# Performance work log

Measured on AMD Instinct MI355X. Metric: run time of the kernel, lower is better.

Reference implementation:

```python
import jax, jax.numpy as jnp
import numpy as np

T, B, IN_DIM, H, NB = 100, 1024, 40, 512, 4
WB, IB, ABMVM, ABNM = 8, 8, 8, 8


def _pact(x, a):
    # PACT clip sign(x)*min(|x|, a); a: (NB,) broadcast over (NB, B, D)
    a = a[:, None, None]
    return jnp.sign(x) * 0.5 * (jnp.abs(x) - jnp.abs(jnp.abs(x) - a) + a)


def _quant(x, bits, rng):
    step = 2.0 ** (bits - 1)
    x01 = jnp.clip(x / rng, -1.0 + 1.0 / step, 1.0 - 1.0 / step)
    return jnp.round(x01 * step) / step * rng


def _q(x, bits, a):
    # straight-through quantizer with per-block range a: (NB,)
    return x + jax.lax.stop_gradient(_quant(x, bits, a[:, None, None]) - x)


@jax.custom_vjp
def custom_mm(x, w, b):
    wc = jnp.clip(w, -1.0, 1.0)
    return jnp.einsum('nbi,nio->nbo', x, _quant(wc, WB, 1.0)) + _quant(b, WB, 1.0)


def _mm_fwd(x, w, b):
    wc = jnp.clip(w, -1.0, 1.0)
    out = jnp.einsum('nbi,nio->nbo', x, _quant(wc, WB, 1.0)) + _quant(b, WB, 1.0)
    return out, (x, wc)


def _mm_bwd(res, g):
    x, wc = res
    return (jnp.einsum('nbo,nio->nbi', g, wc),
            jnp.einsum('nbi,nbo->nio', x, g),
            g.sum(axis=1, keepdims=True))


custom_mm.defvjp(_mm_fwd, _mm_bwd)


def _forward(inputs, weight_ih, weight_hh, bias_ih, bias_hh, a_cell, fc_w, fc_b, fc_a):
    (a1, a2, a3, a4, a5, a6, a7, a8, a9,
     a10, a11, a12, a13, a14) = a_cell
    nb, hd = weight_hh.shape[0], weight_hh.shape[1]
    bsz = inputs.shape[1]

    def step(carry, x_t):
        hx, cx = carry
        xr = jnp.broadcast_to(x_t[None], (nb,) + x_t.shape)  # input.repeat(n_blocks,1,1)
        p1 = custom_mm(_q(_pact(xr, a1), IB, a1), weight_ih, bias_ih)
        p2 = custom_mm(_q(_pact(hx, a11), IB, a11), weight_hh, bias_hh)  # w_mask == ones (drop_p=0)
        pre = _q(_pact(p1, a12), ABMVM, a12) + _q(_pact(p2, a13), ABMVM, a13)
        gates = _q(_pact(pre, a14), ABNM, a14)  # (nb, B, 4H)
        i, j, f, o = jnp.split(gates, 4, axis=2)
        fg = _q(_pact(jax.nn.sigmoid(f), a3), ABNM, a3)
        ig = _q(_pact(jax.nn.sigmoid(i), a4), ABNM, a4)
        jg = _q(_pact(jnp.tanh(j), a5), ABNM, a5)
        og = _q(_pact(jax.nn.sigmoid(o), a6), ABNM, a6)
        gc = _q(_pact(cx * fg, a7), ABNM, a7)
        ai = _q(_pact(ig * jg, a8), ABNM, a8)
        nc = _q(_pact(gc + ai, a9), ABNM, a9)
        ac = _q(_pact(jnp.tanh(nc), a10), ABNM, a10)
        nh = _q(_pact(ac * og, a11), ABNM, a11)
        return (nh, nc), None

    h0 = jnp.zeros((nb, bsz, hd), inputs.dtype)
    (hT, _), _ = jax.lax.scan(step, (h0, h0), inputs)
    fa1, fa2 = fc_a
    fc = _q(_pact(custom_mm(_q(_pact(hT, fa1), IB, fa1), fc_w, fc_b), fa2), ABMVM, fa2)  # (nb, B, 3)
    return fc[:4].transpose(1, 0, 2).reshape(bsz, 12)


def setup_inputs():
    key = jax.random.key(0)
    k = jax.random.split(key, 4)
    lim_ih = 1.0 / np.sqrt(IN_DIM)
    lim_hh = 1.0 / np.sqrt(H)
    lim_fc = np.sqrt(6.0 / H)
    a_vals = jnp.array([128., 16., 1., 1., 1., 1., 4., 1., 4., 1., 4., 4., 4., 4.], jnp.float32)
    return {
        "inputs": jax.random.normal(k[0], (T, B, IN_DIM), jnp.float32),
        "weight_ih": jax.random.uniform(k[1], (NB, IN_DIM, 4 * H), jnp.float32, -lim_ih, lim_ih),
        "weight_hh": jax.random.uniform(k[2], (NB, H, 4 * H), jnp.float32, -lim_hh, lim_hh),
        "bias_ih": jnp.zeros((NB, 1, 4 * H), jnp.float32),
        "bias_hh": jnp.ones((NB, 1, 4 * H), jnp.float32),
        "a_cell": jnp.broadcast_to(a_vals[:, None], (14, NB)),
        "fc_w": jax.random.uniform(k[3], (NB, H, 3), jnp.float32, -lim_fc, lim_fc),
        "fc_b": jnp.zeros((NB, 1, 3), jnp.float32),
        "fc_a": jnp.broadcast_to(jnp.array([4., 16.], jnp.float32)[:, None], (2, NB)),
    }


def reference(inputs, weight_ih, weight_hh, bias_ih, bias_hh, a_cell, fc_w, fc_b, fc_a):
    return _forward(inputs, weight_ih, weight_hh, bias_ih, bias_hh, a_cell, fc_w, fc_b, fc_a)
```

## Files before the change

kernel.cpp:

```cpp
#include <hip/hip_runtime.h>
#include <math.h>

#define T_STEPS 100
#define BATCH   1024
#define INDIM   40
#define HID     512
#define NBLK    4
#define KPAD    576
#define NG      2048
#define LDAP    80

typedef int v4i __attribute__((ext_vector_type(4)));

__device__ __forceinline__ float pact_f(float x, float a){
    float u = fabsf(x);
    float v = fabsf(u - a);
    float s = (x > 0.f) ? 1.f : ((x < 0.f) ? -1.f : 0.f);
    return (s * 0.5f) * ((u - v) + a);
}
__device__ __forceinline__ int quant_int(float x, float inv_a){
    float xs = x * inv_a;
    xs = fminf(fmaxf(xs, -127.f/128.f), 127.f/128.f);
    return (int)rintf(xs * 128.f);
}
__device__ __forceinline__ int clamp127(int v){
    return v > 127 ? 127 : (v < -127 ? -127 : v);
}

__global__ __launch_bounds__(256) void k_quant_x(const float* __restrict__ x,
                                                 signed char* __restrict__ xq){
    int idx = blockIdx.x * 256 + threadIdx.x;
    int k = idx & 63; int tb = idx >> 6;
    signed char q = 0;
    if (k < INDIM){
        float xv = x[tb * INDIM + k];
        float pv = pact_f(xv, 128.f);
        q = (signed char)quant_int(pv, 1.f/128.f);
    }
    xq[idx] = q;
}

__global__ __launch_bounds__(256) void k_quant_w(const float* __restrict__ wih,
                                                 const float* __restrict__ whh,
                                                 signed char* __restrict__ wt){
    int idx = blockIdx.x * 256 + threadIdx.x;
    int kk = idx % KPAD;
    int no = idx / KPAD;
    int c  = no % NG;
    int n  = no / NG;
    int gate = (c >> 4) & 3;
    int h    = ((c >> 6) << 4) | (c & 15);
    int o    = gate * 512 + h;
    float w;
    if (kk < INDIM)      w = wih[((long)n*INDIM + kk)*NG + o];
    else if (kk < 64)    { wt[idx] = 0; return; }
    else                 w = whh[((long)n*HID + (kk-64))*NG + o];
    w = fminf(fmaxf(w, -1.f), 1.f);
    wt[idx] = (signed char)quant_int(w, 1.f);
}

__global__ __launch_bounds__(256) void k_quant_bias(const float* __restrict__ bih,
                                                    const float* __restrict__ bhh,
                                                    int* __restrict__ bihq,
                                                    int* __restrict__ bhhq){
    int idx = blockIdx.x * 256 + threadIdx.x;
    int c = idx % NG; int n = idx / NG;
    int gate = (c >> 4) & 3;
    int h    = ((c >> 6) << 4) | (c & 15);
    int o    = gate * 512 + h;
    bihq[idx] = quant_int(bih[n*NG + o], 1.f);
    bhhq[idx] = quant_int(bhh[n*NG + o], 1.f);
}

__global__ __launch_bounds__(256) void k_quant_fc(const float* __restrict__ fcw,
                                                  const float* __restrict__ fcb,
                                                  signed char* __restrict__ fcwt,
                                                  int* __restrict__ fcbq){
    int idx = blockIdx.x * 256 + threadIdx.x;
    if (idx < NBLK*3*512){
        int k = idx % 512; int nc = idx / 512; int c = nc % 3; int n = nc / 3;
        float w = fcw[((long)n*HID + k)*3 + c];
        w = fminf(fmaxf(w, -1.f), 1.f);
        fcwt[idx] = (signed char)quant_int(w, 1.f);
    }
    if (idx < NBLK*3) fcbq[idx] = quant_int(fcb[idx], 1.f);
}

__global__ void k_luts(signed char* __restrict__ sigl, signed char* __restrict__ thl){
    int i = threadIdx.x;
    if (i < 255){
        double xv = (double)(i - 127) / 32.0;
        float s = (float)(1.0 / (1.0 + exp(-xv)));
        float t = (float)tanh(xv);
        sigl[i] = (signed char)quant_int(pact_f(s, 1.f), 1.f);
        thl[i]  = (signed char)quant_int(pact_f(t, 1.f), 1.f);
    }
}

__global__ __launch_bounds__(256, 2) void k_step(const signed char* __restrict__ xq_t,
                                                 const signed char* __restrict__ Hin,
                                                 signed char* __restrict__ Hout,
                                                 signed char* __restrict__ C,
                                                 const signed char* __restrict__ Wt,
                                                 const int* __restrict__ bihq,
                                                 const int* __restrict__ bhhq,
                                                 const signed char* __restrict__ sigl,
                                                 const signed char* __restrict__ thl){
    __shared__ __align__(16) signed char As[128*LDAP];
    __shared__ __align__(16) signed char Bs[128*LDAP];
    __shared__ signed char s_sig[256], s_th[256];

    int lid = blockIdx.x;
    int swz = (lid & 7) * 64 + (lid >> 3);
    int bm = swz & 7, bn = (swz >> 3) & 15, n = swz >> 7;

    int tid  = threadIdx.x;
    int lane = tid & 63;
    int wave = tid >> 6;
    int wm = wave >> 1, wn = wave & 1;

    if (tid < 255){ s_sig[tid] = sigl[tid]; s_th[tid] = thl[tid]; }

    int hglob = bn*32 + wn*16 + (lane & 15);
    int rbase = bm*128 + wm*64 + ((lane >> 4) << 2);

    int cbase = bn*128 + wn*64 + (lane & 15);
    int b1v[4], b2v[4];
    #pragma unroll
    for (int ni = 0; ni < 4; ++ni){
        int c = cbase + ni*16;
        b1v[ni] = bihq[n*NG + c];
        b2v[ni] = 32 * bhhq[n*NG + c];
    }
    int* Cw = (int*)(C + ((long)(n*HID + hglob))*BATCH + rbase);
    int cold[4];
    #pragma unroll
    for (int mi = 0; mi < 4; ++mi) cold[mi] = Cw[mi*4];

    int sr = tid >> 2;
    int sc = (tid & 3) * 16;
    const signed char* wr0 = Wt  + (long)n*NG*KPAD   + (long)(bn*128 + sr)*KPAD + sc;
    const signed char* wr1 = wr0 + (long)64*KPAD;
    const signed char* hr0 = Hin + (long)n*BATCH*HID + (long)(bm*128 + sr)*HID  + sc;
    const signed char* hr1 = hr0 + (long)64*HID;
    int wlo = sr*LDAP + (tid & 3)*16;
    int whi = wlo + 64*LDAP;

    int4 ra0 = *(const int4*)(xq_t + (long)bm*8192 + tid*16);
    int4 ra1 = *(const int4*)(xq_t + (long)bm*8192 + 4096 + tid*16);
    int4 rb0 = *(const int4*)(wr0);
    int4 rb1 = *(const int4*)(wr1);

    v4i acc1[4][4] = {};
    v4i acc2[4][4] = {};
    int am = wm*64 + (lane & 15);
    int bo = wn*64 + (lane & 15);
    int ak = (lane >> 4) * 16;

    for (int kt = 0; kt < 9; ++kt){
        __syncthreads();
        *(int4*)&As[wlo] = ra0; *(int4*)&As[whi] = ra1;
        *(int4*)&Bs[wlo] = rb0; *(int4*)&Bs[whi] = rb1;
        __syncthreads();
        if (kt < 8){
            ra0 = *(const int4*)(hr0 + kt*64);
            ra1 = *(const int4*)(hr1 + kt*64);
            rb0 = *(const int4*)(wr0 + (kt+1)*64);
            rb1 = *(const int4*)(wr1 + (kt+1)*64);
        }
        v4i af[4], bf[4];
        #pragma unroll
        for (int mi = 0; mi < 4; ++mi) af[mi] = *(const v4i*)&As[(am + mi*16)*LDAP + ak];
        #pragma unroll
        for (int ni = 0; ni < 4; ++ni) bf[ni] = *(const v4i*)&Bs[(bo + ni*16)*LDAP + ak];
        if (kt == 0){
            #pragma unroll
            for (int mi = 0; mi < 4; ++mi)
                #pragma unroll
                for (int ni = 0; ni < 4; ++ni)
                    acc1[mi][ni] = __builtin_amdgcn_mfma_i32_16x16x64_i8(af[mi], bf[ni], acc1[mi][ni], 0, 0, 0);
        } else {
            #pragma unroll
            for (int mi = 0; mi < 4; ++mi)
                #pragma unroll
                for (int ni = 0; ni < 4; ++ni)
                    acc2[mi][ni] = __builtin_amdgcn_mfma_i32_16x16x64_i8(af[mi], bf[ni], acc2[mi][ni], 0, 0, 0);
        }
    }

    long hb = (long)n * BATCH;
    #pragma unroll
    for (int mi = 0; mi < 4; ++mi){
        int cw = cold[mi];
        int cnew = 0;
        #pragma unroll
        for (int r = 0; r < 4; ++r){
            int g4[4];
            #pragma unroll
            for (int ni = 0; ni < 4; ++ni){
                int S1  = acc1[mi][ni][r] + b1v[ni];
                int q12 = clamp127((int)rintf((float)S1 * 0.25f));
                int S2  = acc2[mi][ni][r] + b2v[ni];
                int q13 = clamp127((int)rintf((float)S2 * 0.0078125f));
                g4[ni]  = clamp127(q12 + q13);
            }
            int ig = s_sig[g4[0] + 127];
            int jg = s_th [g4[1] + 127];
            int fg = s_sig[g4[2] + 127];
            int og = s_sig[g4[3] + 127];
            int cc = (signed char)(cw >> (8*r));
            int gc = clamp127((int)rintf((float)(cc * fg) * 0.0078125f));
            int ai = clamp127((int)rintf((float)(ig * jg) * 0.0078125f));
            int nc = clamp127((int)rintf((float)(4*gc + ai) * 0.25f));
            int ac = s_th[nc + 127];
            int nh = clamp127((int)rintf((float)(ac * og) * (1.0f/512.0f)));
            cnew |= (nc & 255) << (8*r);
            Hout[(hb + rbase + mi*16 + r)*HID + hglob] = (signed char)nh;
        }
        Cw[mi*4] = cnew;
    }
}

__global__ __launch_bounds__(256) void k_fc(const signed char* __restrict__ H,
                                            const signed char* __restrict__ fcwt,
                                            const int* __restrict__ fcbq,
                                            float* __restrict__ out){
    int wave = threadIdx.x >> 6, lane = threadIdx.x & 63;
    int nb = blockIdx.x * 4 + wave;
    int n = nb >> 10, b = nb & 1023;
    const signed char* h = H + (long)nb * HID + lane * 8;
    int2 hv = *(const int2*)h;
    int acc[3] = {0, 0, 0};
    #pragma unroll
    for (int c = 0; c < 3; ++c){
        const signed char* wp = fcwt + ((long)(n*3 + c))*512 + lane*8;
        int2 wv = *(const int2*)wp;
        int s = 0;
        #pragma unroll
        for (int e = 0; e < 4; ++e){
            s += (int)(signed char)(hv.x >> (8*e)) * (int)(signed char)(wv.x >> (8*e));
            s += (int)(signed char)(hv.y >> (8*e)) * (int)(signed char)(wv.y >> (8*e));
        }
        acc[c] = s;
    }
    #pragma unroll
    for (int off = 32; off; off >>= 1){
        acc[0] += __shfl_down(acc[0], off, 64);
        acc[1] += __shfl_down(acc[1], off, 64);
        acc[2] += __shfl_down(acc[2], off, 64);
    }
    if (lane == 0){
        #pragma unroll
        for (int c = 0; c < 3; ++c){
            int v = acc[c] + 32 * fcbq[n*3 + c];
            int q = clamp127((int)rintf((float)v * (1.0f/512.0f)));
            out[b*12 + n*3 + c] = (float)q * 0.125f;
        }
    }
}

extern "C" void kernel_launch(void* const* d_in, const int* in_sizes, int n_in,
                              void* d_out, int out_size, void* d_ws, size_t ws_size,
                              hipStream_t stream)
{
    const float* x   = (const float*)d_in[0];
    const float* wih = (const float*)d_in[1];
    const float* whh = (const float*)d_in[2];
    const float* bih = (const float*)d_in[3];
    const float* bhh = (const float*)d_in[4];
    const float* fcw = (const float*)d_in[6];
    const float* fcb = (const float*)d_in[7];
    float* out = (float*)d_out;
    (void)in_sizes; (void)n_in; (void)out_size; (void)ws_size;

    char* p = (char*)d_ws;
    auto alloc = [&](size_t nbytes){ char* r = p; p += (nbytes + 255) & ~(size_t)255; return r; };
    signed char* Xq   = (signed char*)alloc((size_t)T_STEPS*BATCH*64);
    signed char* Wt   = (signed char*)alloc((size_t)NBLK*NG*KPAD);
    signed char* Hb0  = (signed char*)alloc((size_t)NBLK*BATCH*HID);
    signed char* Hb1  = (signed char*)alloc((size_t)NBLK*BATCH*HID);
    signed char* Cb   = (signed char*)alloc((size_t)NBLK*BATCH*HID);
    int*         bihq = (int*)alloc((size_t)NBLK*NG*4);
    int*         bhhq = (int*)alloc((size_t)NBLK*NG*4);
    signed char* fcwt = (signed char*)alloc((size_t)NBLK*3*512);
    int*         fcbq = (int*)alloc((size_t)NBLK*3*4);
    signed char* sigl = (signed char*)alloc(256);
    signed char* thl  = (signed char*)alloc(256);

    k_quant_x   <<<(T_STEPS*BATCH*64)/256, 256, 0, stream>>>(x, Xq);
    k_quant_w   <<<(NBLK*NG*KPAD)/256,     256, 0, stream>>>(wih, whh, Wt);
    k_quant_bias<<<(NBLK*NG)/256,          256, 0, stream>>>(bih, bhh, bihq, bhhq);
    k_quant_fc  <<<(NBLK*3*512)/256,       256, 0, stream>>>(fcw, fcb, fcwt, fcbq);
    k_luts      <<<1, 256, 0, stream>>>(sigl, thl);
    hipMemsetAsync(Hb0, 0, (size_t)3*NBLK*BATCH*HID, stream);

    for (int t = 0; t < T_STEPS; ++t){
        const signed char* Hi = (t & 1) ? Hb1 : Hb0;
        signed char*       Ho = (t & 1) ? Hb0 : Hb1;
        k_step<<<512, 256, 0, stream>>>(Xq + (size_t)t*BATCH*64, Hi, Ho, Cb, Wt, bihq, bhhq, sigl, thl);
    }
    k_fc<<<(NBLK*BATCH)/4, 256, 0, stream>>>(Hb0, fcwt, fcbq, out);
}
```

Measured before the change: 1.428 ms.

## Replace per-timestep launches with persistent kernel holding weights in LDS and grid barrier

Replaces the 100 per-timestep kernel launches with one persistent kernel of 256 blocks. Each block loads its 128-column weight panel into shared memory once, keeps the cell state in registers instead of global memory, and synchronises timesteps with a global atomic counter barrier. This removes launch overhead, the repeated weight reloads and the C-state round trips. In exchange it depends on all 256 blocks being co-resident for the spin barrier and uses about 117KB of LDS per block. The H tile is double-buffered in LDS.

```diff
diff --git a/kernel.cpp b/kernel.cpp
--- a/kernel.cpp
+++ b/kernel.cpp
@@ -9,6 +9,10 @@
 #define KPAD    576
 #define NG      2048
 #define LDAP    80
+#define LDWP    592
+#define SMEM_WS 75776
+#define SMEM_AS 20480
+#define SMEM_TOTAL (SMEM_WS + 2*SMEM_AS + 512)
 
 typedef int v4i __attribute__((ext_vector_type(4)));
 
@@ -97,127 +101,169 @@
     }
 }
 
-__global__ __launch_bounds__(256, 2) void k_step(const signed char* __restrict__ xq_t,
-                                                 const signed char* __restrict__ Hin,
-                                                 signed char* __restrict__ Hout,
-                                                 signed char* __restrict__ C,
-                                                 const signed char* __restrict__ Wt,
-                                                 const int* __restrict__ bihq,
-                                                 const int* __restrict__ bhhq,
-                                                 const signed char* __restrict__ sigl,
-                                                 const signed char* __restrict__ thl){
-    __shared__ __align__(16) signed char As[128*LDAP];
-    __shared__ __align__(16) signed char Bs[128*LDAP];
-    __shared__ signed char s_sig[256], s_th[256];
-
-    int lid = blockIdx.x;
-    int swz = (lid & 7) * 64 + (lid >> 3);
-    int bm = swz & 7, bn = (swz >> 3) & 15, n = swz >> 7;
+__global__ __launch_bounds__(512, 2) void k_persist(const signed char* __restrict__ Xq,
+                                                    signed char* __restrict__ H0,
+                                                    signed char* __restrict__ H1,
+                                                    const signed char* __restrict__ Wt,
+                                                    const int* __restrict__ bihq,
+                                                    const int* __restrict__ bhhq,
+                                                    const signed char* __restrict__ sigl,
+                                                    const signed char* __restrict__ thl,
+                                                    unsigned int* __restrict__ bar){
+    extern __shared__ char smem[];
+    signed char* Ws    = (signed char*)smem;
+    signed char* As    = (signed char*)(smem + SMEM_WS);
+    signed char* s_sig = (signed char*)(smem + SMEM_WS + 2*SMEM_AS);
+    signed char* s_th  = s_sig + 256;
 
     int tid  = threadIdx.x;
     int lane = tid & 63;
     int wave = tid >> 6;
     int wm = wave >> 1, wn = wave & 1;
 
+    int bid  = blockIdx.x;
+    int xcd  = bid & 7, slot = bid >> 3;
+    int gidx = xcd * 2 + (slot >> 4);
+    int n    = gidx >> 2;
+    int bmq  = gidx & 3;
+    int bn   = slot & 15;
+
+    const signed char* wpan = Wt + ((long)n*NG + (long)bn*128) * KPAD;
+    for (int i = tid; i < 4608; i += 512){
+        int row = i / 36, c = (i % 36) * 16;
+        *(int4*)&Ws[row*LDWP + c] = *(const int4*)(wpan + (long)row*KPAD + c);
+    }
     if (tid < 255){ s_sig[tid] = sigl[tid]; s_th[tid] = thl[tid]; }
 
     int hglob = bn*32 + wn*16 + (lane & 15);
-    int rbase = bm*128 + wm*64 + ((lane >> 4) << 2);
-
+    int rbase = bmq*256 + wm*64 + ((lane >> 4) << 2);
     int cbase = bn*128 + wn*64 + (lane & 15);
     int b1v[4], b2v[4];
     #pragma unroll
     for (int ni = 0; ni < 4; ++ni){
-        int c = cbase + ni*16;
-        b1v[ni] = bihq[n*NG + c];
-        b2v[ni] = 32 * bhhq[n*NG + c];
-    }
-    int* Cw = (int*)(C + ((long)(n*HID + hglob))*BATCH + rbase);
-    int cold[4];
-    #pragma unroll
-    for (int mi = 0; mi < 4; ++mi) cold[mi] = Cw[mi*4];
-
-    int sr = tid >> 2;
-    int sc = (tid & 3) * 16;
-    const signed char* wr0 = Wt  + (long)n*NG*KPAD   + (long)(bn*128 + sr)*KPAD + sc;
-    const signed char* wr1 = wr0 + (long)64*KPAD;
-    const signed char* hr0 = Hin + (long)n*BATCH*HID + (long)(bm*128 + sr)*HID  + sc;
-    const signed char* hr1 = hr0 + (long)64*HID;
-    int wlo = sr*LDAP + (tid & 3)*16;
-    int whi = wlo + 64*LDAP;
-
-    int4 ra0 = *(const int4*)(xq_t + (long)bm*8192 + tid*16);
-    int4 ra1 = *(const int4*)(xq_t + (long)bm*8192 + 4096 + tid*16);
-    int4 rb0 = *(const int4*)(wr0);
-    int4 rb1 = *(const int4*)(wr1);
-
-    v4i acc1[4][4] = {};
-    v4i acc2[4][4] = {};
+        b1v[ni] = bihq[n*NG + cbase + ni*16];
+        b2v[ni] = 32 * bhhq[n*NG + cbase + ni*16];
+    }
+    int cold[4] = {0,0,0,0};
+
+    int  srow = tid >> 1;
+    int  scol = (tid & 1) * 32;
+    int  aoff = srow*LDAP + scol;
+    long hoff = ((long)(n*BATCH + bmq*256 + srow)) * HID + scol;
+    const signed char* xb = Xq + (long)bmq*16384 + srow*64 + scol;
+
     int am = wm*64 + (lane & 15);
-    int bo = wn*64 + (lane & 15);
     int ak = (lane >> 4) * 16;
-
-    for (int kt = 0; kt < 9; ++kt){
+    int bro = (wn*64 + (lane & 15)) * LDWP;
+
+    __syncthreads();
+
+    for (int t = 0; t < T_STEPS; ++t){
+        const signed char* Hin  = (t & 1) ? H1 : H0;
+        signed char*       Hout = (t & 1) ? H0 : H1;
+
+        const signed char* xp = xb + (long)t * (BATCH*64);
+        int4 rx0 = *(const int4*)xp;
+        int4 rx1 = *(const int4*)(xp + 16);
+
+        if (t){
+            __syncthreads();
+            if (tid == 0){
+                __builtin_amdgcn_fence(__ATOMIC_RELEASE, "agent");
+                atomicAdd(bar, 1u);
+                unsigned tgt = (unsigned)t * 256u;
+                while (__hip_atomic_load(bar, __ATOMIC_RELAXED, __HIP_MEMORY_SCOPE_AGENT) < tgt)
+                    __builtin_amdgcn_s_sleep(1);
+                __builtin_amdgcn_fence(__ATOMIC_ACQUIRE, "agent");
+            }
+            __syncthreads();
+        }
+
+        *(int4*)&As[aoff] = rx0; *(int4*)&As[aoff + 16] = rx1;
         __syncthreads();
-        *(int4*)&As[wlo] = ra0; *(int4*)&As[whi] = ra1;
-        *(int4*)&Bs[wlo] = rb0; *(int4*)&Bs[whi] = rb1;
-        __syncthreads();
-        if (kt < 8){
-            ra0 = *(const int4*)(hr0 + kt*64);
-            ra1 = *(const int4*)(hr1 + kt*64);
-            rb0 = *(const int4*)(wr0 + (kt+1)*64);
-            rb1 = *(const int4*)(wr1 + (kt+1)*64);
-        }
-        v4i af[4], bf[4];
-        #pragma unroll
-        for (int mi = 0; mi < 4; ++mi) af[mi] = *(const v4i*)&As[(am + mi*16)*LDAP + ak];
-        #pragma unroll
-        for (int ni = 0; ni < 4; ++ni) bf[ni] = *(const v4i*)&Bs[(bo + ni*16)*LDAP + ak];
-        if (kt == 0){
+        int4 ha0 = *(const int4*)(Hin + hoff);
+        int4 ha1 = *(const int4*)(Hin + hoff + 16);
+        int4 hb0 = *(const int4*)(Hin + hoff + 64);
+        int4 hb1 = *(const int4*)(Hin + hoff + 80);
+
+        v4i acc1[4][4] = {};
+        {
+            v4i af[4], bf[4];
+            #pragma unroll
+            for (int mi = 0; mi < 4; ++mi) af[mi] = *(const v4i*)&As[(am + mi*16)*LDAP + ak];
+            #pragma unroll
+            for (int ni = 0; ni < 4; ++ni) bf[ni] = *(const v4i*)&Ws[bro + ni*16*LDWP + ak];
             #pragma unroll
             for (int mi = 0; mi < 4; ++mi)
                 #pragma unroll
                 for (int ni = 0; ni < 4; ++ni)
                     acc1[mi][ni] = __builtin_amdgcn_mfma_i32_16x16x64_i8(af[mi], bf[ni], acc1[mi][ni], 0, 0, 0);
-        } else {
+        }
+        int q12p[4][4];
+        #pragma unroll
+        for (int mi = 0; mi < 4; ++mi)
+            #pragma unroll
+            for (int ni = 0; ni < 4; ++ni){
+                int p = 0;
+                #pragma unroll
+                for (int r = 0; r < 4; ++r){
+                    int q = clamp127((int)rintf((float)(acc1[mi][ni][r] + b1v[ni]) * 0.25f));
+                    p |= (q & 255) << (8*r);
+                }
+                q12p[mi][ni] = p;
+            }
+
+        v4i acc2[4][4] = {};
+        for (int kt = 1; kt <= 8; ++kt){
+            signed char* Ab = As + (kt & 1) * SMEM_AS;
+            *(int4*)&Ab[aoff] = ha0; *(int4*)&Ab[aoff + 16] = ha1;
+            __syncthreads();
+            ha0 = hb0; ha1 = hb1;
+            if (kt <= 6){
+                hb0 = *(const int4*)(Hin + hoff + (kt+1)*64);
+                hb1 = *(const int4*)(Hin + hoff + (kt+1)*64 + 16);
+            }
+            v4i af[4], bf[4];
+            #pragma unroll
+            for (int mi = 0; mi < 4; ++mi) af[mi] = *(const v4i*)&Ab[(am + mi*16)*LDAP + ak];
+            #pragma unroll
+            for (int ni = 0; ni < 4; ++ni) bf[ni] = *(const v4i*)&Ws[bro + ni*16*LDWP + kt*64 + ak];
             #pragma unroll
             for (int mi = 0; mi < 4; ++mi)
                 #pragma unroll
                 for (int ni = 0; ni < 4; ++ni)
                     acc2[mi][ni] = __builtin_amdgcn_mfma_i32_16x16x64_i8(af[mi], bf[ni], acc2[mi][ni], 0, 0, 0);
         }
-    }
-
-    long hb = (long)n * BATCH;
-    #pragma unroll
-    for (int mi = 0; mi < 4; ++mi){
-        int cw = cold[mi];
-        int cnew = 0;
+
         #pragma unroll
-        for (int r = 0; r < 4; ++r){
-            int g4[4];
-            #pragma unroll
-            for (int ni = 0; ni < 4; ++ni){
-                int S1  = acc1[mi][ni][r] + b1v[ni];
-                int q12 = clamp127((int)rintf((float)S1 * 0.25f));
-                int S2  = acc2[mi][ni][r] + b2v[ni];
-                int q13 = clamp127((int)rintf((float)S2 * 0.0078125f));
-                g4[ni]  = clamp127(q12 + q13);
+        for (int mi = 0; mi < 4; ++mi){
+            int cw = cold[mi];
+            int cnew = 0;
+            #pragma unroll
+            for (int r = 0; r < 4; ++r){
+                int g4[4];
+                #pragma unroll
+                for (int ni = 0; ni < 4; ++ni){
+                    int S2  = acc2[mi][ni][r] + b2v[ni];
+                    int q13 = clamp127((int)rintf((float)S2 * 0.0078125f));
+                    int q12 = (signed char)(q12p[mi][ni] >> (8*r));
+                    g4[ni]  = clamp127(q12 + q13);
+                }
+                int ig = s_sig[g4[0] + 127];
+                int jg = s_th [g4[1] + 127];
+                int fg = s_sig[g4[2] + 127];
+                int og = s_sig[g4[3] + 127];
+                int cc = (signed char)(cw >> (8*r));
+                int gc = clamp127((int)rintf((float)(cc * fg) * 0.0078125f));
+                int ai = clamp127((int)rintf((float)(ig * jg) * 0.0078125f));
+                int nc = clamp127((int)rintf((float)(4*gc + ai) * 0.25f));
+                int ac = s_th[nc + 127];
+                int nh = clamp127((int)rintf((float)(ac * og) * (1.0f/512.0f)));
+                cnew |= (nc & 255) << (8*r);
+                Hout[((long)(n*BATCH) + rbase + mi*16 + r)*HID + hglob] = (signed char)nh;
             }
-            int ig = s_sig[g4[0] + 127];
-            int jg = s_th [g4[1] + 127];
-            int fg = s_sig[g4[2] + 127];
-            int og = s_sig[g4[3] + 127];
-            int cc = (signed char)(cw >> (8*r));
-            int gc = clamp127((int)rintf((float)(cc * fg) * 0.0078125f));
-            int ai = clamp127((int)rintf((float)(ig * jg) * 0.0078125f));
-            int nc = clamp127((int)rintf((float)(4*gc + ai) * 0.25f));
-            int ac = s_th[nc + 127];
-            int nh = clamp127((int)rintf((float)(ac * og) * (1.0f/512.0f)));
-            cnew |= (nc & 255) << (8*r);
-            Hout[(hb + rbase + mi*16 + r)*HID + hglob] = (signed char)nh;
-        }
-        Cw[mi*4] = cnew;
+            cold[mi] = cnew;
+        }
     }
 }
 
@@ -279,25 +325,25 @@
     signed char* Wt   = (signed char*)alloc((size_t)NBLK*NG*KPAD);
     signed char* Hb0  = (signed char*)alloc((size_t)NBLK*BATCH*HID);
     signed char* Hb1  = (signed char*)alloc((size_t)NBLK*BATCH*HID);
-    signed char* Cb   = (signed char*)alloc((size_t)NBLK*BATCH*HID);
     int*         bihq = (int*)alloc((size_t)NBLK*NG*4);
     int*         bhhq = (int*)alloc((size_t)NBLK*NG*4);
     signed char* fcwt = (signed char*)alloc((size_t)NBLK*3*512);
     int*         fcbq = (int*)alloc((size_t)NBLK*3*4);
     signed char* sigl = (signed char*)alloc(256);
     signed char* thl  = (signed char*)alloc(256);
+    unsigned*    bar  = (unsigned*)alloc(256);
+
+    hipFuncSetAttribute((const void*)k_persist,
+                        hipFuncAttributeMaxDynamicSharedMemorySize, SMEM_TOTAL);
 
     k_quant_x   <<<(T_STEPS*BATCH*64)/256, 256, 0, stream>>>(x, Xq);
     k_quant_w   <<<(NBLK*NG*KPAD)/256,     256, 0, stream>>>(wih, whh, Wt);
     k_quant_bias<<<(NBLK*NG)/256,          256, 0, stream>>>(bih, bhh, bihq, bhhq);
     k_quant_fc  <<<(NBLK*3*512)/256,       256, 0, stream>>>(fcw, fcb, fcwt, fcbq);
     k_luts      <<<1, 256, 0, stream>>>(sigl, thl);
-    hipMemsetAsync(Hb0, 0, (size_t)3*NBLK*BATCH*HID, stream);
-
-    for (int t = 0; t < T_STEPS; ++t){
-        const signed char* Hi = (t & 1) ? Hb1 : Hb0;
-        signed char*       Ho = (t & 1) ? Hb0 : Hb1;
-        k_step<<<512, 256, 0, stream>>>(Xq + (size_t)t*BATCH*64, Hi, Ho, Cb, Wt, bihq, bhhq, sigl, thl);
-    }
+    hipMemsetAsync(Hb0, 0, (size_t)NBLK*BATCH*HID, stream);
+    hipMemsetAsync(bar, 0, 256, stream);
+
+    k_persist<<<256, 512, SMEM_TOTAL, stream>>>(Xq, Hb0, Hb1, Wt, bihq, bhhq, sigl, thl, bar);
     k_fc<<<(NBLK*BATCH)/4, 256, 0, stream>>>(Hb0, fcwt, fcbq, out);
 }
```

Measured after the change: 2.387 ms. +67.1%, slower.

## Double-buffer LDS tiles, pack early input-gate quantization, remap blocks per XCD

Applied to the files above, without the earlier changes.

Shared-memory A/W tiles are double-buffered, which removes one __syncthreads per K iteration. The global-to-shared load pattern changes to two 16-byte chunks per thread over 128 rows. The input-projection accumulator is quantized and packed into bytes right after the first K tile, freeing 64 accumulator registers for the rest of the loop. Block-to-tile mapping is changed so each XCD pair handles one block-diagonal n, improving L2 reuse of weights, at the cost of doubled LDS use that may lower occupancy.

```diff
diff --git a/kernel.cpp b/kernel.cpp
--- a/kernel.cpp
+++ b/kernel.cpp
@@ -106,13 +106,16 @@
                                                  const int* __restrict__ bhhq,
                                                  const signed char* __restrict__ sigl,
                                                  const signed char* __restrict__ thl){
-    __shared__ __align__(16) signed char As[128*LDAP];
-    __shared__ __align__(16) signed char Bs[128*LDAP];
+    __shared__ __align__(16) signed char As[2][128*LDAP];
+    __shared__ __align__(16) signed char Ws[2][128*LDAP];
     __shared__ signed char s_sig[256], s_th[256];
 
-    int lid = blockIdx.x;
-    int swz = (lid & 7) * 64 + (lid >> 3);
-    int bm = swz & 7, bn = (swz >> 3) & 15, n = swz >> 7;
+    int bid = blockIdx.x;
+    int xcd = bid & 7, slot = bid >> 3;
+    int n   = xcd >> 1;
+    int idx = ((xcd & 1) << 6) | slot;
+    int bm  = idx & 7;
+    int bn  = idx >> 3;
 
     int tid  = threadIdx.x;
     int lane = tid & 63;
@@ -123,62 +126,73 @@
 
     int hglob = bn*32 + wn*16 + (lane & 15);
     int rbase = bm*128 + wm*64 + ((lane >> 4) << 2);
-
     int cbase = bn*128 + wn*64 + (lane & 15);
     int b1v[4], b2v[4];
     #pragma unroll
     for (int ni = 0; ni < 4; ++ni){
-        int c = cbase + ni*16;
-        b1v[ni] = bihq[n*NG + c];
-        b2v[ni] = 32 * bhhq[n*NG + c];
+        b1v[ni] = bihq[n*NG + cbase + ni*16];
+        b2v[ni] = 32 * bhhq[n*NG + cbase + ni*16];
     }
     int* Cw = (int*)(C + ((long)(n*HID + hglob))*BATCH + rbase);
     int cold[4];
     #pragma unroll
     for (int mi = 0; mi < 4; ++mi) cold[mi] = Cw[mi*4];
 
-    int sr = tid >> 2;
-    int sc = (tid & 3) * 16;
-    const signed char* wr0 = Wt  + (long)n*NG*KPAD   + (long)(bn*128 + sr)*KPAD + sc;
-    const signed char* wr1 = wr0 + (long)64*KPAD;
-    const signed char* hr0 = Hin + (long)n*BATCH*HID + (long)(bm*128 + sr)*HID  + sc;
-    const signed char* hr1 = hr0 + (long)64*HID;
-    int wlo = sr*LDAP + (tid & 3)*16;
-    int whi = wlo + 64*LDAP;
-
-    int4 ra0 = *(const int4*)(xq_t + (long)bm*8192 + tid*16);
-    int4 ra1 = *(const int4*)(xq_t + (long)bm*8192 + 4096 + tid*16);
-    int4 rb0 = *(const int4*)(wr0);
-    int4 rb1 = *(const int4*)(wr1);
-
-    v4i acc1[4][4] = {};
-    v4i acc2[4][4] = {};
+    int  srow = tid >> 1;
+    int  scol = (tid & 1) * 32;
+    int  aoff = srow*LDAP + scol;
+    const signed char* hrow = Hin + ((long)(n*BATCH + bm*128 + srow))*HID + scol;
+    const signed char* wrow = Wt  + ((long)n*NG + bn*128 + srow)*KPAD + scol;
+
     int am = wm*64 + (lane & 15);
     int bo = wn*64 + (lane & 15);
     int ak = (lane >> 4) * 16;
 
+    const signed char* xrow = xq_t + (bm*128 + srow)*64 + scol;
+    int4 ra0 = *(const int4*)xrow;
+    int4 ra1 = *(const int4*)(xrow + 16);
+    int4 rw0 = *(const int4*)wrow;
+    int4 rw1 = *(const int4*)(wrow + 16);
+
+    v4i acc1[4][4] = {};
+    v4i acc2[4][4] = {};
+    int q12p[4][4];
+
     for (int kt = 0; kt < 9; ++kt){
-        __syncthreads();
-        *(int4*)&As[wlo] = ra0; *(int4*)&As[whi] = ra1;
-        *(int4*)&Bs[wlo] = rb0; *(int4*)&Bs[whi] = rb1;
+        signed char* Ab = As[kt & 1];
+        signed char* Wb = Ws[kt & 1];
+        *(int4*)&Ab[aoff] = ra0; *(int4*)&Ab[aoff + 16] = ra1;
+        *(int4*)&Wb[aoff] = rw0; *(int4*)&Wb[aoff + 16] = rw1;
         __syncthreads();
         if (kt < 8){
-            ra0 = *(const int4*)(hr0 + kt*64);
-            ra1 = *(const int4*)(hr1 + kt*64);
-            rb0 = *(const int4*)(wr0 + (kt+1)*64);
-            rb1 = *(const int4*)(wr1 + (kt+1)*64);
+            ra0 = *(const int4*)(hrow + kt*64);
+            ra1 = *(const int4*)(hrow + kt*64 + 16);
+            rw0 = *(const int4*)(wrow + (kt+1)*64);
+            rw1 = *(const int4*)(wrow + (kt+1)*64 + 16);
         }
         v4i af[4], bf[4];
         #pragma unroll
-        for (int mi = 0; mi < 4; ++mi) af[mi] = *(const v4i*)&As[(am + mi*16)*LDAP + ak];
-        #pragma unroll
-        for (int ni = 0; ni < 4; ++ni) bf[ni] = *(const v4i*)&Bs[(bo + ni*16)*LDAP + ak];
+        for (int mi = 0; mi < 4; ++mi) af[mi] = *(const v4i*)&Ab[(am + mi*16)*LDAP + ak];
+        #pragma unroll
+        for (int ni = 0; ni < 4; ++ni) bf[ni] = *(const v4i*)&Wb[(bo + ni*16)*LDAP + ak];
         if (kt == 0){
             #pragma unroll
             for (int mi = 0; mi < 4; ++mi)
                 #pragma unroll
                 for (int ni = 0; ni < 4; ++ni)
                     acc1[mi][ni] = __builtin_amdgcn_mfma_i32_16x16x64_i8(af[mi], bf[ni], acc1[mi][ni], 0, 0, 0);
+            #pragma unroll
+            for (int mi = 0; mi < 4; ++mi)
+                #pragma unroll
+                for (int ni = 0; ni < 4; ++ni){
+                    int pk = 0;
+                    #pragma unroll
+                    for (int r = 0; r < 4; ++r){
+                        int q = clamp127((int)rintf((float)(acc1[mi][ni][r] + b1v[ni]) * 0.25f));
+                        pk |= (q & 255) << (8*r);
+                    }
+                    q12p[mi][ni] = pk;
+                }
         } else {
             #pragma unroll
             for (int mi = 0; mi < 4; ++mi)
@@ -188,7 +202,6 @@
         }
     }
 
-    long hb = (long)n * BATCH;
     #pragma unroll
     for (int mi = 0; mi < 4; ++mi){
         int cw = cold[mi];
@@ -198,10 +211,9 @@
             int g4[4];
             #pragma unroll
             for (int ni = 0; ni < 4; ++ni){
-                int S1  = acc1[mi][ni][r] + b1v[ni];
-                int q12 = clamp127((int)rintf((float)S1 * 0.25f));
                 int S2  = acc2[mi][ni][r] + b2v[ni];
                 int q13 = clamp127((int)rintf((float)S2 * 0.0078125f));
+                int q12 = (signed char)(q12p[mi][ni] >> (8*r));
                 g4[ni]  = clamp127(q12 + q13);
             }
             int ig = s_sig[g4[0] + 127];
@@ -215,7 +227,7 @@
             int ac = s_th[nc + 127];
             int nh = clamp127((int)rintf((float)(ac * og) * (1.0f/512.0f)));
             cnew |= (nc & 255) << (8*r);
-            Hout[(hb + rbase + mi*16 + r)*HID + hglob] = (signed char)nh;
+            Hout[((long)(n*BATCH) + rbase + mi*16 + r)*HID + hglob] = (signed char)nh;
         }
         Cw[mi*4] = cnew;
     }
```

After: 1.263 ms. -11.5%, faster.
